# Kernel optimization log

Hardware: AMD Instinct MI355X
Metric: run time of the kernel (lower is better)

The kernel has to match this reference:

```python
import jax, jax.numpy as jnp
import numpy as np

GROUPS = 32
EPS = 1e-6

def group_norm(x, gamma, beta):
    # x: [B,C,H,W]
    B, C, H, W = x.shape
    xg = x.reshape(B, GROUPS, C // GROUPS, H, W)
    mu = xg.mean(axis=(2, 3, 4), keepdims=True)
    var = xg.var(axis=(2, 3, 4), keepdims=True)
    xn = ((xg - mu) * jax.lax.rsqrt(var + EPS)).reshape(B, C, H, W)
    return xn * gamma[None, :, None, None] + beta[None, :, None, None]

def setup_inputs() -> dict:
    key = jax.random.key(0)
    ks = jax.random.split(key, 12)
    B, C, H, W = 4, 256, 64, 64
    s = 1.0 / np.sqrt(C)
    return {
        "x": jax.random.normal(ks[0], (B, C, H, W), jnp.float32),
        "gn_gamma": jnp.ones((C,), jnp.float32),
        "gn_beta": jnp.zeros((C,), jnp.float32),
        "wq": jax.random.normal(ks[1], (C, C), jnp.float32) * s,
        "bq": jnp.zeros((C,), jnp.float32),
        "wk": jax.random.normal(ks[2], (C, C), jnp.float32) * s,
        "bk": jnp.zeros((C,), jnp.float32),
        "wv": jax.random.normal(ks[3], (C, C), jnp.float32) * s,
        "bv": jnp.zeros((C,), jnp.float32),
        "wu": jax.random.normal(ks[4], (1, C), jnp.float32) * s,
        "bu": jnp.zeros((1,), jnp.float32),
        "wp": jax.random.normal(ks[5], (C, C), jnp.float32) * s,
        "bp": jnp.zeros((C,), jnp.float32),
    }

def reference(x, gn_gamma, gn_beta, wq, bq, wk, bk, wv, bv, wu, bu, wp, bp):
    B, C, H, W = x.shape
    hw = H * W
    hn = group_norm(x, gn_gamma, gn_beta)          # norm(x); context=x so same norm
    t = hn.reshape(B, C, hw).transpose(0, 2, 1)    # [B, hw, C]
    q = t @ wq.T + bq                              # 1x1 conv == per-token linear
    k = t @ wk.T + bk
    v = t @ wv.T + bv
    u_map = jax.nn.sigmoid(t @ wu.T + bu)          # [B, hw, 1]
    scale = jnp.asarray(C, x.dtype) ** -0.5
    scores = jnp.einsum('bic,bjc->bij', q, k) * scale * u_map.transpose(0, 2, 1)
    attn = jax.nn.softmax(scores, axis=2)          # softmax over keys j
    out = jnp.einsum('bij,bjc->bic', attn, v)      # [B, hw, C]
    out = (out @ wp.T + bp).transpose(0, 2, 1).reshape(B, C, H, W)
    return (x + out, u_map)
```

## Files before the change

kernel.cpp:

```cpp
#include <hip/hip_runtime.h>
#include <cstdint>

#define B_ 4
#define C_ 256
#define HW_ 4096
#define CPG_ 8
#define M_TOT 16384
#define SCALE 0.0625f
#define LOG2E 1.44269504088896f
#define FLASH_LDS 133120

typedef __attribute__((ext_vector_type(4))) float f32x4;
typedef __attribute__((ext_vector_type(16))) float f32x16;
typedef __attribute__((ext_vector_type(8))) unsigned short u16x8;
typedef __attribute__((ext_vector_type(4))) unsigned short u16x4;
typedef __attribute__((ext_vector_type(4))) unsigned int u32x4;
typedef __attribute__((ext_vector_type(8))) __bf16 bf16x8;

static __device__ __forceinline__ unsigned short f2bf(float f) {
  unsigned int u = __builtin_bit_cast(unsigned int, f);
  u += 0x7fffu + ((u >> 16) & 1u);
  return (unsigned short)(u >> 16);
}
static __device__ __forceinline__ float bf2f(unsigned short s) {
  return __builtin_bit_cast(float, ((unsigned int)s) << 16);
}
static __device__ __forceinline__ bf16x8 ldbf8(const unsigned short* p) {
  return __builtin_bit_cast(bf16x8, *(const u16x8*)p);
}
static __device__ __forceinline__ bf16x8 cvt8(const float* p) {
  f32x4 a = *(const f32x4*)p;
  f32x4 b = *(const f32x4*)(p + 4);
  u16x8 r;
  r[0] = f2bf(a[0]); r[1] = f2bf(a[1]); r[2] = f2bf(a[2]); r[3] = f2bf(a[3]);
  r[4] = f2bf(b[0]); r[5] = f2bf(b[1]); r[6] = f2bf(b[2]); r[7] = f2bf(b[3]);
  return __builtin_bit_cast(bf16x8, r);
}
static __device__ __forceinline__ void gload16(const void* g, void* l) {
  __builtin_amdgcn_global_load_lds(
      (const __attribute__((address_space(1))) unsigned int*)g,
      (__attribute__((address_space(3))) unsigned int*)l, 16, 0, 0);
}
static __device__ __forceinline__ unsigned cvtpk(float lo, float hi) {
  unsigned r;
  asm("v_cvt_pk_bf16_f32 %0, %1, %2" : "=v"(r) : "v"(lo), "v"(hi));
  return r;
}

__global__ __launch_bounds__(256) void gn_stats(const float* __restrict__ x,
    const float* __restrict__ gamma, const float* __restrict__ beta,
    float* __restrict__ gnab) {
  int bg = blockIdx.x;
  int b = bg >> 5, g = bg & 31;
  const float* xp = x + ((size_t)(b * C_ + g * CPG_)) * HW_;
  float s = 0.f, ss = 0.f;
  for (int i = threadIdx.x; i < CPG_ * HW_; i += 256) {
    float v = xp[i]; s += v; ss += v * v;
  }
#pragma unroll
  for (int m = 32; m; m >>= 1) { s += __shfl_xor(s, m); ss += __shfl_xor(ss, m); }
  __shared__ float red[8];
  if ((threadIdx.x & 63) == 0) { red[threadIdx.x >> 6] = s; red[4 + (threadIdx.x >> 6)] = ss; }
  __syncthreads();
  if (threadIdx.x < CPG_) {
    float S = red[0] + red[1] + red[2] + red[3];
    float SS = red[4] + red[5] + red[6] + red[7];
    float mean = S * (1.f / 32768.f);
    float var = SS * (1.f / 32768.f) - mean * mean;
    float rs = rsqrtf(var + 1e-6f);
    int c = g * CPG_ + threadIdx.x;
    float gm = gamma[c];
    gnab[b * C_ + c] = gm * rs;
    gnab[1024 + b * C_ + c] = beta[c] - mean * gm * rs;
  }
}

__global__ __launch_bounds__(256) void gn_apply(const float* __restrict__ x,
    const float* __restrict__ gnab, unsigned short* __restrict__ t) {
  __shared__ unsigned short T[64][264];
  int blk = blockIdx.x;
  int b = blk >> 6;
  int sp0 = (blk & 63) * 64;
  int tid = threadIdx.x;
  int l = tid & 63, w = tid >> 6;
  const float* xb = x + (size_t)b * C_ * HW_;
  const float* ga = gnab + b * C_;
  const float* gb = gnab + 1024 + b * C_;
  for (int c0 = w * 64; c0 < w * 64 + 64; c0 += 8) {
    u16x8 o;
#pragma unroll
    for (int j = 0; j < 8; ++j) {
      int c = c0 + j;
      float v = xb[(size_t)c * HW_ + sp0 + l];
      o[j] = f2bf(v * ga[c] + gb[c]);
    }
    *(u16x8*)&T[l][c0] = o;
  }
  __syncthreads();
  for (int e = tid; e < 64 * 32; e += 256) {
    int row = e >> 5, c8 = (e & 31) * 8;
    *(u16x8*)(t + ((size_t)(b * HW_ + sp0 + row)) * C_ + c8) =
        *(const u16x8*)&T[row][c8];
  }
}

__global__ __launch_bounds__(256) void u_kernel(const unsigned short* __restrict__ t,
    const float* __restrict__ wu, const float* __restrict__ bu,
    float* __restrict__ uout) {
  int w = threadIdx.x >> 6, l = threadIdx.x & 63;
  int tok = blockIdx.x * 4 + w;
  u16x4 tv = *(const u16x4*)(t + (size_t)tok * C_ + l * 4);
  f32x4 wv4 = *(const f32x4*)(wu + l * 4);
  float d = bf2f(tv[0]) * wv4[0] + bf2f(tv[1]) * wv4[1] +
            bf2f(tv[2]) * wv4[2] + bf2f(tv[3]) * wv4[3];
#pragma unroll
  for (int m = 32; m; m >>= 1) d += __shfl_xor(d, m);
  if (l == 0) uout[tok] = 1.f / (1.f + __expf(-(d + bu[0])));
}

__global__ __launch_bounds__(256, 2) void qkv_kernel(const unsigned short* __restrict__ t,
    const float* __restrict__ wq, const float* __restrict__ wk, const float* __restrict__ wv,
    const float* __restrict__ bq, const float* __restrict__ bk, const float* __restrict__ bv,
    const float* __restrict__ uu,
    unsigned short* __restrict__ q, unsigned short* __restrict__ k,
    unsigned short* __restrict__ vt) {
  int mblk = blockIdx.x, nblk = blockIdx.y;
  int n0 = nblk * 64;
  __shared__ unsigned short WL[64][264];
  __shared__ float lds[64][65];
  int tid = threadIdx.x;
  int wid = tid >> 6, l = tid & 63;
  int lr = l & 15, lg = l >> 4;
  int row = mblk * 64 + wid * 16 + lr;
  bf16x8 af[8];
  const unsigned short* ap = t + (size_t)row * C_ + lg * 8;
#pragma unroll
  for (int kc = 0; kc < 8; ++kc) af[kc] = ldbf8(ap + kc * 32);
  f32x4 u4 = *(const f32x4*)(uu + mblk * 64 + wid * 16 + lg * 4);

#pragma unroll 1
  for (int w = 0; w < 3; ++w) {
    const float* W = w == 0 ? wq : (w == 1 ? wk : wv);
    const float* bias = w == 0 ? bq : (w == 1 ? bk : bv);
    if (w) __syncthreads();
#pragma unroll
    for (int p = 0; p < 8; ++p) {
      int rw = p * 8 + (tid >> 5);
      int kc0 = (tid & 31) * 8;
      *(bf16x8*)&WL[rw][kc0] = cvt8(W + (size_t)(n0 + rw) * C_ + kc0);
    }
    __syncthreads();
    f32x4 acc[4] = {};
#pragma unroll
    for (int kc = 0; kc < 8; ++kc)
#pragma unroll
      for (int j = 0; j < 4; ++j) {
        bf16x8 bb = ldbf8(&WL[j * 16 + lr][kc * 32 + lg * 8]);
        acc[j] = __builtin_amdgcn_mfma_f32_16x16x32_bf16(af[kc], bb, acc[j], 0, 0, 0);
      }
    if (w < 2) {
      unsigned short* dst = w ? k : q;
      float su[4] = {1.f, 1.f, 1.f, 1.f};
      if (w == 1) {
        su[0] = SCALE * LOG2E * u4[0]; su[1] = SCALE * LOG2E * u4[1];
        su[2] = SCALE * LOG2E * u4[2]; su[3] = SCALE * LOG2E * u4[3];
      }
#pragma unroll
      for (int j = 0; j < 4; ++j) {
        int col = n0 + j * 16 + lr;
        float bv_ = bias[col];
#pragma unroll
        for (int r = 0; r < 4; ++r)
          dst[(size_t)(mblk * 64 + wid * 16 + lg * 4 + r) * C_ + col] =
              f2bf((acc[j][r] + bv_) * su[r]);
      }
    } else {
#pragma unroll
      for (int j = 0; j < 4; ++j) {
        float bv_ = bias[n0 + j * 16 + lr];
#pragma unroll
        for (int r = 0; r < 4; ++r)
          lds[wid * 16 + lg * 4 + r][j * 16 + lr] = acc[j][r] + bv_;
      }
      __syncthreads();
      int bb_ = (mblk * 64) >> 12;
      int s0 = (mblk * 64) & 4095;
      int ss = tid & 63, cc0 = tid >> 6;
      for (int cc = cc0; cc < 64; cc += 4)
        vt[((size_t)(bb_ * C_ + n0 + cc)) * HW_ + s0 + ss] = f2bf(lds[ss][cc]);
    }
  }
}

__global__ __launch_bounds__(512, 2) void flash_kernel(const unsigned short* __restrict__ q,
    const unsigned short* __restrict__ k, const unsigned short* __restrict__ vt,
    unsigned short* __restrict__ o) {
  extern __shared__ char smem[];
  float* cmb_m = (float*)(smem + 131072);
  float* cmb_l = (float*)(smem + 131584);
  float* facw  = (float*)(smem + 132096);
  float* scrL  = (float*)(smem + 132608);

  int blk = blockIdx.x;
  int b = blk >> 6;
  int qrow0 = (blk & 63) * 64;
  int tid = threadIdx.x;
  int wid = tid >> 6, l = tid & 63;
  int l5 = l & 31, hi = l >> 5;

  const unsigned short* kb = k + (size_t)b * HW_ * C_;
  const unsigned short* vb = vt + (size_t)b * C_ * HW_;

  float mrow = -1e30f, lrow = 0.f;
  f32x16 oa[8];

  if (wid >= 4) {
    int role = wid - 4;
    int sh = role & 1;
    bool isK = role < 2;
    int w_ = l >> 2;
    int w0_ = w_ & 1, w1_ = (w_ >> 1) & 1, w2_ = (w_ >> 2) & 1, w3_ = (w_ >> 3) & 1;
    int koffb = (l & 3) * 8;
#define STG(IT, BUFN)                                                           \
    {                                                                           \
      int key0n = sh * 2048 + (IT) * 32;                                        \
      if (isK) {                                                                \
        _Pragma("unroll")                                                       \
        for (int j = 0; j < 16; ++j) {                                          \
          int key = j * 2 + hi;                                                 \
          const unsigned short* g =                                             \
              kb + (size_t)(key0n + key) * C_ + ((l5 * 8) ^ (key * 8));         \
          gload16(g, smem + (BUFN) * 32768 + sh * 16384 + j * 1024);            \
        }                                                                       \
      } else {                                                                  \
        _Pragma("unroll")                                                       \
        for (int j = 0; j < 16; ++j) {                                          \
          int j0 = j & 1;                                                       \
          int ch = (j << 4) | (w3_ << 3) | ((w2_ ^ j0) << 2) |                  \
                   ((w1_ ^ w3_) << 1) | (w0_ ^ w2_ ^ j0);                       \
          int ke = koffb ^ ((ch & 3) << 3);                                     \
          const unsigned short* g = vb + (size_t)ch * HW_ + key0n + ke;         \
          gload16(g, smem + 65536 + (BUFN) * 32768 + sh * 16384 + j * 1024);    \
        }                                                                       \
      }                                                                         \
    }
    STG(0, 0);
    __syncthreads();
    for (int it = 0; it < 64; ++it) {
      if (it + 1 < 64) STG(it + 1, (it + 1) & 1);
      __syncthreads();
    }
#undef STG
  } else {
    int h = wid >> 1, qs = wid & 1;
    bf16x8 qreg[16];
    {
      const unsigned short* qp =
          q + ((size_t)b * HW_ + qrow0 + qs * 32 + l5) * C_ + hi * 8;
#pragma unroll
      for (int cc = 0; cc < 16; ++cc) qreg[cc] = ldbf8(qp + cc * 16);
    }
#pragma unroll
    for (int ct = 0; ct < 8; ++ct)
#pragma unroll
      for (int r = 0; r < 16; ++r) oa[ct][r] = 0.f;
    __syncthreads();

    int kx = l5 << 4;
    int vbase = (l5 * 64) ^ ((l5 >> 2) << 6);
    int ko0 = (hi * 16) ^ ((l & 3) << 4);
    int ko1 = (32 + hi * 16) ^ ((l & 3) << 4);

    for (int it = 0; it < 64; ++it) {
      int buf = it & 1;
      const char* KB = smem + buf * 32768 + h * 16384;
      f32x16 s;
#pragma unroll
      for (int r = 0; r < 16; ++r) s[r] = 0.f;
#pragma unroll
      for (int cc = 0; cc < 16; ++cc) {
        bf16x8 kf = ldbf8((const unsigned short*)(KB + l5 * 512 +
                                                  ((cc * 32 + hi * 16) ^ kx)));
        s = __builtin_amdgcn_mfma_f32_32x32x16_bf16(kf, qreg[cc], s, 0, 0, 0);
      }
      float a0 = fmaxf(s[0], s[1]),   a1 = fmaxf(s[2], s[3]);
      float a2 = fmaxf(s[4], s[5]),   a3 = fmaxf(s[6], s[7]);
      float a4 = fmaxf(s[8], s[9]),   a5 = fmaxf(s[10], s[11]);
      float a6 = fmaxf(s[12], s[13]), a7 = fmaxf(s[14], s[15]);
      float b0 = fmaxf(fmaxf(a0, a1), fmaxf(a2, a3));
      float b1 = fmaxf(fmaxf(a4, a5), fmaxf(a6, a7));
      float mxl = fmaxf(b0, b1);
      float mx = fmaxf(mxl, __shfl_xor(mxl, 32));
      if (!__all(mx <= mrow + 11.f)) {
        float mnew = fmaxf(mrow, mx);
        float scr = exp2f(mrow - mnew);
        mrow = mnew;
        lrow *= scr;
        if (hi == 0) scrL[wid * 32 + l5] = scr;
        float sr[16];
#pragma unroll
        for (int r = 0; r < 16; ++r)
          sr[r] = scrL[wid * 32 + (r & 3) + 8 * (r >> 2) + 4 * hi];
#pragma unroll
        for (int ct = 0; ct < 8; ++ct)
#pragma unroll
          for (int r = 0; r < 16; ++r) oa[ct][r] *= sr[r];
      }
      unsigned wp[8];
#pragma unroll
      for (int rp = 0; rp < 8; ++rp) {
        float e0 = exp2f(s[2 * rp] - mrow);
        float e1 = exp2f(s[2 * rp + 1] - mrow);
        lrow += e0 + e1;
        wp[rp] = cvtpk(e0, e1);
      }
      unsigned sx[8];
#pragma unroll
      for (int rp = 0; rp < 8; ++rp) sx[rp] = (unsigned)__shfl_xor((int)wp[rp], 32);
      bool hib = (hi != 0);
      u32x4 pa0u = {hib ? sx[2] : wp[0], hib ? sx[3] : wp[1],
                    hib ? wp[2] : sx[0], hib ? wp[3] : sx[1]};
      u32x4 pa1u = {hib ? sx[6] : wp[4], hib ? sx[7] : wp[5],
                    hib ? wp[6] : sx[4], hib ? wp[7] : sx[5]};
      bf16x8 pa0 = __builtin_bit_cast(bf16x8, pa0u);
      bf16x8 pa1 = __builtin_bit_cast(bf16x8, pa1u);
      const char* VB = smem + 65536 + buf * 32768 + h * 16384;
#pragma unroll
      for (int ct = 0; ct < 8; ++ct) {
        bf16x8 v0 = ldbf8((const unsigned short*)(VB + ct * 2048 + vbase + ko0));
        bf16x8 v1 = ldbf8((const unsigned short*)(VB + ct * 2048 + vbase + ko1));
        oa[ct] = __builtin_amdgcn_mfma_f32_32x32x16_bf16(pa0, v0, oa[ct], 0, 0, 0);
        oa[ct] = __builtin_amdgcn_mfma_f32_32x32x16_bf16(pa1, v1, oa[ct], 0, 0, 0);
      }
      __syncthreads();
    }
  }

  float l_all = 0.f;
  if (wid < 4) {
    l_all = lrow + __shfl_xor(lrow, 32);
    if (hi == 0) { cmb_m[wid * 32 + l5] = mrow; cmb_l[wid * 32 + l5] = l_all; }
  }
  __syncthreads();
  if (wid < 4) {
    float mo = cmb_m[(wid ^ 2) * 32 + l5];
    float lo = cmb_l[(wid ^ 2) * 32 + l5];
    float M = fmaxf(mrow, mo);
    float el = exp2f(mrow - M), eo = exp2f(mo - M);
    float fac = el / (l_all * el + lo * eo);
    if (hi == 0) facw[wid * 32 + l5] = fac;
    float fr[16];
#pragma unroll
    for (int r = 0; r < 16; ++r)
      fr[r] = facw[wid * 32 + (r & 3) + 8 * (r >> 2) + 4 * hi];
    float* Ow = (float*)(smem + wid * 32768);
#pragma unroll
    for (int ct = 0; ct < 8; ++ct)
#pragma unroll
      for (int r = 0; r < 16; ++r) {
        int qr = (r & 3) + 8 * (r >> 2) + 4 * hi;
        Ow[qr * 256 + ct * 32 + l5] = oa[ct][r] * fr[r];
      }
  }
  __syncthreads();
  for (int e = tid; e < 2048; e += 512) {
    int row = e >> 5;
    int c8 = (e & 31) * 8;
    int qs_ = row >> 5, q_ = row & 31;
    const float* p0 = (const float*)(smem + qs_ * 32768) + q_ * 256 + c8;
    const float* p1 = (const float*)(smem + (2 + qs_) * 32768) + q_ * 256 + c8;
    u16x8 ov;
#pragma unroll
    for (int j = 0; j < 8; ++j) ov[j] = f2bf(p0[j] + p1[j]);
    *(u16x8*)(o + ((size_t)b * HW_ + qrow0 + row) * C_ + c8) = ov;
  }
}

__global__ __launch_bounds__(256, 2) void proj_kernel(const unsigned short* __restrict__ o,
    const float* __restrict__ wp, const float* __restrict__ bp,
    const float* __restrict__ x, float* __restrict__ y) {
  int mblk = blockIdx.x, nblk = blockIdx.y;
  int n0 = nblk * 64;
  __shared__ unsigned short WL[64][264];
  int tid = threadIdx.x;
#pragma unroll
  for (int p = 0; p < 8; ++p) {
    int row = p * 8 + (tid >> 5);
    int kc0 = (tid & 31) * 8;
    *(bf16x8*)&WL[row][kc0] = cvt8(wp + (size_t)(n0 + row) * C_ + kc0);
  }
  __syncthreads();
  int wid = tid >> 6, l = tid & 63;
  int lr = l & 15, lg = l >> 4;
  int row = mblk * 64 + wid * 16 + lr;
  f32x4 acc[4] = {};
  const unsigned short* ap = o + (size_t)row * C_ + lg * 8;
#pragma unroll
  for (int kc = 0; kc < 8; ++kc) {
    bf16x8 a = ldbf8(ap + kc * 32);
#pragma unroll
    for (int j = 0; j < 4; ++j) {
      bf16x8 bb = ldbf8(&WL[j * 16 + lr][kc * 32 + lg * 8]);
      acc[j] = __builtin_amdgcn_mfma_f32_16x16x32_bf16(a, bb, acc[j], 0, 0, 0);
    }
  }
  __shared__ float lds[64][65];
#pragma unroll
  for (int j = 0; j < 4; ++j) {
    float bv_ = bp[n0 + j * 16 + lr];
#pragma unroll
    for (int r = 0; r < 4; ++r)
      lds[wid * 16 + lg * 4 + r][j * 16 + lr] = acc[j][r] + bv_;
  }
  __syncthreads();
  int bb_ = (mblk * 64) >> 12;
  int s0 = (mblk * 64) & 4095;
  int ss = tid & 63, cc0 = tid >> 6;
  for (int cc = cc0; cc < 64; cc += 4) {
    size_t idx = ((size_t)(bb_ * C_ + n0 + cc)) * HW_ + s0 + ss;
    y[idx] = x[idx] + lds[ss][cc];
  }
}

extern "C" void kernel_launch(void* const* d_in, const int* in_sizes, int n_in,
                              void* d_out, int out_size, void* d_ws, size_t ws_size,
                              hipStream_t stream) {
  const float* x     = (const float*)d_in[0];
  const float* gamma = (const float*)d_in[1];
  const float* beta  = (const float*)d_in[2];
  const float* wq    = (const float*)d_in[3];
  const float* bq    = (const float*)d_in[4];
  const float* wk    = (const float*)d_in[5];
  const float* bk    = (const float*)d_in[6];
  const float* wv    = (const float*)d_in[7];
  const float* bv    = (const float*)d_in[8];
  const float* wu    = (const float*)d_in[9];
  const float* bu    = (const float*)d_in[10];
  const float* wp    = (const float*)d_in[11];
  const float* bp    = (const float*)d_in[12];

  float* y = (float*)d_out;
  float* uout = y + (size_t)B_ * C_ * HW_;

  unsigned short* t  = (unsigned short*)d_ws;
  unsigned short* qb = t + (size_t)M_TOT * C_;
  unsigned short* kk = qb + (size_t)M_TOT * C_;
  unsigned short* vt = kk + (size_t)M_TOT * C_;

  hipFuncSetAttribute((const void*)flash_kernel,
                      hipFuncAttributeMaxDynamicSharedMemorySize, FLASH_LDS);

  gn_stats<<<128, 256, 0, stream>>>(x, gamma, beta, uout);
  gn_apply<<<256, 256, 0, stream>>>(x, uout, t);
  u_kernel<<<4096, 256, 0, stream>>>(t, wu, bu, uout);
  qkv_kernel<<<dim3(256, 4), 256, 0, stream>>>(t, wq, wk, wv, bq, bk, bv, uout, qb, kk, vt);
  flash_kernel<<<256, 512, FLASH_LDS, stream>>>(qb, kk, vt, t);
  proj_kernel<<<dim3(256, 4), 256, 0, stream>>>(t, wp, bp, x, y);
}
```

Baseline: 188.2 us.

## Double query rows per flash block to share staged K/V across eight compute waves

The flash attention block grows from 64 to 128 query rows. It now has 8 compute waves (4 query slices times 2 key halves) plus the same 4 loader waves, 768 threads in all, and the grid is halved. Each K/V tile staged in LDS is therefore reused by twice as many query rows, which halves global K/V traffic and the number of staging passes. The final combine of the two key halves now accumulates in place in one fp32 LDS buffer over two phases with an extra barrier. Only one block of 768 threads fits per CU given the LDS size, so 128 blocks cover just half of the mi355x's 256 CUs. That cuts parallelism and may offset the reuse gain.

```diff
diff --git a/kernel.cpp b/kernel.cpp
--- a/kernel.cpp
+++ b/kernel.cpp
@@ -8,7 +8,7 @@
 #define M_TOT 16384
 #define SCALE 0.0625f
 #define LOG2E 1.44269504088896f
-#define FLASH_LDS 133120
+#define FLASH_LDS 135168
 
 typedef __attribute__((ext_vector_type(4))) float f32x4;
 typedef __attribute__((ext_vector_type(16))) float f32x16;
@@ -192,18 +192,19 @@
   }
 }
 
-__global__ __launch_bounds__(512, 2) void flash_kernel(const unsigned short* __restrict__ q,
+__global__ __launch_bounds__(768, 3) void flash_kernel(const unsigned short* __restrict__ q,
     const unsigned short* __restrict__ k, const unsigned short* __restrict__ vt,
     unsigned short* __restrict__ o) {
   extern __shared__ char smem[];
   float* cmb_m = (float*)(smem + 131072);
-  float* cmb_l = (float*)(smem + 131584);
-  float* facw  = (float*)(smem + 132096);
-  float* scrL  = (float*)(smem + 132608);
+  float* cmb_l = (float*)(smem + 132096);
+  float* facw  = (float*)(smem + 133120);
+  float* scrL  = (float*)(smem + 134144);
+  float* Oacc  = (float*)smem;
 
   int blk = blockIdx.x;
-  int b = blk >> 6;
-  int qrow0 = (blk & 63) * 64;
+  int b = blk >> 5;
+  int qrow0 = (blk & 31) * 128;
   int tid = threadIdx.x;
   int wid = tid >> 6, l = tid & 63;
   int l5 = l & 31, hi = l >> 5;
@@ -211,11 +212,12 @@
   const unsigned short* kb = k + (size_t)b * HW_ * C_;
   const unsigned short* vb = vt + (size_t)b * C_ * HW_;
 
-  float mrow = -1e30f, lrow = 0.f;
+  float mrow = -1e30f, lrow = 0.f, l_all = 0.f;
   f32x16 oa[8];
-
-  if (wid >= 4) {
-    int role = wid - 4;
+  int h = wid >> 2, qs = wid & 3;
+
+  if (wid >= 8) {
+    int role = wid - 8;
     int sh = role & 1;
     bool isK = role < 2;
     int w_ = l >> 2;
@@ -252,7 +254,6 @@
     }
 #undef STG
   } else {
-    int h = wid >> 1, qs = wid & 1;
     bf16x8 qreg[16];
     {
       const unsigned short* qp =
@@ -334,44 +335,55 @@
       }
       __syncthreads();
     }
-  }
-
-  float l_all = 0.f;
-  if (wid < 4) {
     l_all = lrow + __shfl_xor(lrow, 32);
     if (hi == 0) { cmb_m[wid * 32 + l5] = mrow; cmb_l[wid * 32 + l5] = l_all; }
   }
-  __syncthreads();
-  if (wid < 4) {
-    float mo = cmb_m[(wid ^ 2) * 32 + l5];
-    float lo = cmb_l[(wid ^ 2) * 32 + l5];
+
+  __syncthreads();
+  float fac = 0.f;
+  if (wid < 8) {
+    float mo = cmb_m[(wid ^ 4) * 32 + l5];
+    float lo = cmb_l[(wid ^ 4) * 32 + l5];
     float M = fmaxf(mrow, mo);
     float el = exp2f(mrow - M), eo = exp2f(mo - M);
-    float fac = el / (l_all * el + lo * eo);
+    fac = el / (l_all * el + lo * eo);
     if (hi == 0) facw[wid * 32 + l5] = fac;
+  }
+  if (wid < 8 && h == 0) {
     float fr[16];
 #pragma unroll
     for (int r = 0; r < 16; ++r)
       fr[r] = facw[wid * 32 + (r & 3) + 8 * (r >> 2) + 4 * hi];
-    float* Ow = (float*)(smem + wid * 32768);
 #pragma unroll
     for (int ct = 0; ct < 8; ++ct)
 #pragma unroll
       for (int r = 0; r < 16; ++r) {
         int qr = (r & 3) + 8 * (r >> 2) + 4 * hi;
-        Ow[qr * 256 + ct * 32 + l5] = oa[ct][r] * fr[r];
-      }
-  }
-  __syncthreads();
-  for (int e = tid; e < 2048; e += 512) {
+        Oacc[(qs * 32 + qr) * 256 + ct * 32 + l5] = oa[ct][r] * fr[r];
+      }
+  }
+  __syncthreads();
+  if (wid < 8 && h == 1) {
+    float fr[16];
+#pragma unroll
+    for (int r = 0; r < 16; ++r)
+      fr[r] = facw[wid * 32 + (r & 3) + 8 * (r >> 2) + 4 * hi];
+#pragma unroll
+    for (int ct = 0; ct < 8; ++ct)
+#pragma unroll
+      for (int r = 0; r < 16; ++r) {
+        int qr = (r & 3) + 8 * (r >> 2) + 4 * hi;
+        Oacc[(qs * 32 + qr) * 256 + ct * 32 + l5] += oa[ct][r] * fr[r];
+      }
+  }
+  __syncthreads();
+  for (int e = tid; e < 128 * 32; e += 768) {
     int row = e >> 5;
     int c8 = (e & 31) * 8;
-    int qs_ = row >> 5, q_ = row & 31;
-    const float* p0 = (const float*)(smem + qs_ * 32768) + q_ * 256 + c8;
-    const float* p1 = (const float*)(smem + (2 + qs_) * 32768) + q_ * 256 + c8;
+    const float* p = Oacc + row * 256 + c8;
     u16x8 ov;
 #pragma unroll
-    for (int j = 0; j < 8; ++j) ov[j] = f2bf(p0[j] + p1[j]);
+    for (int j = 0; j < 8; ++j) ov[j] = f2bf(p[j]);
     *(u16x8*)(o + ((size_t)b * HW_ + qrow0 + row) * C_ + c8) = ov;
   }
 }
@@ -454,6 +466,6 @@
   gn_apply<<<256, 256, 0, stream>>>(x, uout, t);
   u_kernel<<<4096, 256, 0, stream>>>(t, wu, bu, uout);
   qkv_kernel<<<dim3(256, 4), 256, 0, stream>>>(t, wq, wk, wv, bq, bk, bv, uout, qb, kk, vt);
-  flash_kernel<<<256, 512, FLASH_LDS, stream>>>(qb, kk, vt, t);
+  flash_kernel<<<128, 768, FLASH_LDS, stream>>>(qb, kk, vt, t);
   proj_kernel<<<dim3(256, 4), 256, 0, stream>>>(t, wp, bp, x, y);
 }
```

After: 504.1 us. +167.8%, slower.
